# Kernel optimization log

Measured on AMD Instinct MI355X. Metric: run time of the kernel, lower is better.

The kernel has to match this reference:

```python
import jax, jax.numpy as jnp
import numpy as np

G = 64  # voxel grid extent per axis; grid_ind entries are in [0, G)


def setup_inputs() -> dict:
    key = jax.random.key(0)
    k1, k2 = jax.random.split(key)
    N = 4_000_000
    points = jax.random.normal(k1, (N, 7), dtype=jnp.float32)
    grid_ind = jax.random.randint(k2, (N, 3), 0, G, dtype=jnp.int64)
    return {"points": points, "grid_ind": grid_ind}


def reference(points, grid_ind):
    # torch.unique(grid_ind, dim=0, return_inverse=True) sorts rows
    # lexicographically; for nonnegative coords that equals sorting the
    # linearized index, so we dedup the linear id instead of rows.
    N = points.shape[0]
    gi = grid_ind.astype(jnp.int32)
    lin = (gi[:, 0] * G + gi[:, 1]) * G + gi[:, 2]  # [N]
    # fixed-size unique for jit compatibility: at most N unique voxels,
    # padded with fill_value=-1 at the tail.
    unq, unq_inv = jnp.unique(lin, return_inverse=True, size=N, fill_value=-1)
    # scatter_mean over point->voxel mapping
    sums = jax.ops.segment_sum(points, unq_inv, num_segments=N)          # [N, 7]
    cnt = jax.ops.segment_sum(jnp.ones((N,), points.dtype), unq_inv,
                              num_segments=N)                            # [N]
    mean = sums / jnp.maximum(cnt, 1.0)[:, None]
    # reconstruct the [n_unique_padded, 3] voxel coordinates (pad rows = -1)
    valid = unq >= 0
    u = jnp.maximum(unq, 0)
    unq3 = jnp.stack([u // (G * G), (u // G) % G, u % G], axis=-1)
    unq3 = jnp.where(valid[:, None], unq3, -1).astype(grid_ind.dtype)
    return mean, unq3
```

## Files before the change

### kernel.cpp

```cpp
#include <hip/hip_runtime.h>

#define NVOX 262144
#define NB   256
#define VPB  1024
#define PPB  2048
#define SCT  512
#define NBLK 256

__global__ void dv_fill(const unsigned* __restrict__ nuP,
                        float* __restrict__ out, int n) {
    int nu = (int)*nuP;
    size_t meanChunks = (size_t)n * 7 / 4;
    size_t coordChunks = (size_t)n * 3 / 4;
    size_t total = meanChunks + coordChunks;
    size_t i = (size_t)blockIdx.x * blockDim.x + threadIdx.x;
    if (i >= total) return;
    float* mean = out;
    float* coords = out + (size_t)n * 7;
    if (i < meanChunks) {
        size_t base = i * 4, lim = (size_t)nu * 7;
        if (base >= lim) {
            *(float4*)(mean + base) = make_float4(0.f, 0.f, 0.f, 0.f);
        } else if (base + 4 > lim) {
            for (size_t k = lim; k < base + 4; ++k) mean[k] = 0.f;
        }
    } else {
        size_t base = (i - meanChunks) * 4, lim = (size_t)nu * 3;
        if (base >= lim) {
            *(float4*)(coords + base) = make_float4(-1.f, -1.f, -1.f, -1.f);
        } else if (base + 4 > lim) {
            for (size_t k = lim; k < base + 4; ++k) coords[k] = -1.f;
        }
    }
}

__device__ __forceinline__ unsigned bf16rne(float x) {
    unsigned u = __float_as_uint(x);
    u += 0x7fffu + ((u >> 16) & 1u);
    return u >> 16;
}

__global__ void __launch_bounds__(SCT) rx_scatfuse(
        const int* __restrict__ gi, const float* __restrict__ pts, int n,
        unsigned* __restrict__ cursor, int capb, uint4* __restrict__ recs) {
    __shared__ uint4 recS[PPB];
    __shared__ unsigned dstS[PPB];
    __shared__ unsigned hist[NB];
    __shared__ unsigned bStart[NB];
    __shared__ unsigned runS[NB];
    int t = threadIdx.x, b = blockIdx.x;
    int base = b * PPB;
    int cnt = n - base;
    if (cnt > PPB) cnt = PPB;
    if (t < NB) hist[t] = 0;
    __syncthreads();

    unsigned keyA[PPB / SCT], rankA[PPB / SCT];
    int p0 = base + t * 4;
    if (p0 + 4 <= n) {
        const int4* g4 = (const int4*)(gi + (size_t)base * 3);
        int4 a = g4[3 * t], c = g4[3 * t + 1], d = g4[3 * t + 2];
        keyA[0] = ((unsigned)((a.x << 2) | (a.y >> 4)) << 10) |
                  (unsigned)(((a.y & 15) << 6) | a.z);
        keyA[1] = ((unsigned)((a.w << 2) | (c.x >> 4)) << 10) |
                  (unsigned)(((c.x & 15) << 6) | c.y);
        keyA[2] = ((unsigned)((c.z << 2) | (c.w >> 4)) << 10) |
                  (unsigned)(((c.w & 15) << 6) | d.x);
        keyA[3] = ((unsigned)((d.y << 2) | (d.z >> 4)) << 10) |
                  (unsigned)(((d.z & 15) << 6) | d.w);
#pragma unroll
        for (int j = 0; j < 4; ++j)
            rankA[j] = atomicAdd(&hist[keyA[j] >> 10], 1u);
    } else {
#pragma unroll
        for (int j = 0; j < 4; ++j) {
            int i = p0 + j;
            if (i < n) {
                int g0 = gi[3 * i], g1 = gi[3 * i + 1], g2 = gi[3 * i + 2];
                keyA[j] = ((unsigned)((g0 << 2) | (g1 >> 4)) << 10) |
                          (unsigned)(((g1 & 15) << 6) | g2);
                rankA[j] = atomicAdd(&hist[keyA[j] >> 10], 1u);
            }
        }
    }
    __syncthreads();
    unsigned mine = (t < NB) ? hist[t] : 0u;
    for (int d = 1; d < NB; d <<= 1) {
        unsigned v = (t < NB && t >= d) ? hist[t - d] : 0u;
        __syncthreads();
        if (t < NB) hist[t] += v;
        __syncthreads();
    }
    if (t < NB) {
        bStart[t] = hist[t] - mine;
        runS[t] = (mine > 0) ? atomicAdd(&cursor[t], mine) : 0u;
    }
    __syncthreads();

#pragma unroll
    for (int j = 0; j < PPB / SCT; ++j) {
        int lid = t * 4 + j;
        if (lid < cnt) {
            int i = base + lid;
            const float* p = pts + (size_t)i * 7;
            float f0 = p[0], f1 = p[1], f2 = p[2], f3 = p[3];
            float f4 = p[4], f5 = p[5], f6 = p[6];
            unsigned key = keyA[j], rank = rankA[j];
            unsigned bk = key >> 10, sub = key & 1023u;
            uint4 r;
            r.x = bf16rne(f0) | (bf16rne(f1) << 16);
            r.y = bf16rne(f2) | (bf16rne(f3) << 16);
            r.z = bf16rne(f4) | (bf16rne(f5) << 16);
            r.w = bf16rne(f6) | (sub << 16);
            unsigned sp = bStart[bk] + rank;
            recS[sp] = r;
            dstS[sp] = (unsigned)bk * (unsigned)capb + runS[bk] + rank;
        }
    }
    __syncthreads();
#pragma unroll
    for (int k = 0; k < PPB / SCT; ++k) {
        int j = k * SCT + t;
        if (j < cnt) recs[dstS[j]] = recS[j];
    }
}

__global__ void rx_scan256(const unsigned* __restrict__ in,
                           unsigned* __restrict__ out) {
    __shared__ unsigned sm[NB];
    int t = threadIdx.x;
    unsigned mine = in[t];
    sm[t] = mine;
    __syncthreads();
    for (int off = 1; off < NB; off <<= 1) {
        unsigned v = (t >= off) ? sm[t - off] : 0u;
        __syncthreads();
        sm[t] += v;
        __syncthreads();
    }
    out[t] = sm[t] - mine;
    if (t == NB - 1) out[NB] = sm[t];
}

__global__ void __launch_bounds__(1024) rx_accum(
        const uint4* __restrict__ recs, const unsigned* __restrict__ cursor,
        int capb, float* __restrict__ accTable,
        unsigned* __restrict__ occCount) {
    __shared__ uint4 sortedR[2048];
    __shared__ unsigned cnt_[VPB];
    __shared__ unsigned wsum[16];
    int t = threadIdx.x, bk = blockIdx.x;
    int lane = t & 63, wid = t >> 6;
    unsigned len = cursor[bk];
    size_t base = (size_t)bk * (unsigned)capb;
    float a0 = 0.f, a1 = 0.f, a2 = 0.f, a3 = 0.f,
          a4 = 0.f, a5 = 0.f, a6 = 0.f, cf = 0.f;
    for (unsigned cs = 0; cs < len; cs += 2048) {
        bool v0 = (cs + t) < len, v1 = (cs + 1024 + t) < len;
        uint4 r0, r1;
        unsigned k0 = 0, k1 = 0, rk0 = 0, rk1 = 0;
        if (v0) { r0 = recs[base + cs + t]; k0 = r0.w >> 16; }
        if (v1) { r1 = recs[base + cs + 1024 + t]; k1 = r1.w >> 16; }
        cnt_[t] = 0;
        __syncthreads();
        if (v0) rk0 = atomicAdd(&cnt_[k0], 1u);
        if (v1) rk1 = atomicAdd(&cnt_[k1], 1u);
        __syncthreads();
        unsigned own = cnt_[t];
        unsigned x = own;
#pragma unroll
        for (int d = 1; d < 64; d <<= 1) {
            unsigned y = __shfl_up(x, d, 64);
            if (lane >= d) x += y;
        }
        if (lane == 63) wsum[wid] = x;
        __syncthreads();
        if (t < 64) {
            unsigned w = (lane < 16) ? wsum[lane] : 0u;
            unsigned xx = w;
#pragma unroll
            for (int d = 1; d < 16; d <<= 1) {
                unsigned y = __shfl_up(xx, d, 64);
                if (lane >= d) xx += y;
            }
            if (lane < 16) wsum[lane] = xx - w;
        }
        __syncthreads();
        unsigned excl = x - own + wsum[wid];
        cnt_[t] = excl;
        __syncthreads();
        if (v0) sortedR[cnt_[k0] + rk0] = r0;
        if (v1) sortedR[cnt_[k1] + rk1] = r1;
        __syncthreads();
        unsigned st = excl, end = excl + own;
        for (unsigned k = st; k < end; ++k) {
            uint4 r = sortedR[k];
            a0 += __uint_as_float(r.x << 16);
            a1 += __uint_as_float(r.x & 0xffff0000u);
            a2 += __uint_as_float(r.y << 16);
            a3 += __uint_as_float(r.y & 0xffff0000u);
            a4 += __uint_as_float(r.z << 16);
            a5 += __uint_as_float(r.z & 0xffff0000u);
            a6 += __uint_as_float(r.w << 16);
            cf += 1.f;
        }
        __syncthreads();
    }
    float4* o = (float4*)(accTable + ((size_t)bk * VPB + t) * 8);
    o[0] = make_float4(a0, a1, a2, a3);
    o[1] = make_float4(a4, a5, a6, cf);
    unsigned long long m = __ballot(cf > 0.f);
    if (lane == 0) wsum[wid] = (unsigned)__popcll(m);
    __syncthreads();
    if (t == 0) {
        unsigned occ = 0;
#pragma unroll
        for (int w = 0; w < 16; ++w) occ += wsum[w];
        occCount[bk] = occ;
    }
}

__global__ void rx_emit(const float* __restrict__ accTable,
                        const unsigned* __restrict__ rankBase,
                        float* __restrict__ out_mean,
                        float* __restrict__ out_coords) {
    int bk = blockIdx.x, t = threadIdx.x;
    float row[4][8];
    int pre[4], mycount = 0;
#pragma unroll
    for (int j = 0; j < 4; ++j) {
        int v = t * 4 + j;
        const float4* a = (const float4*)(accTable + ((size_t)bk * VPB + v) * 8);
        float4 r0 = a[0], r1 = a[1];
        row[j][0] = r0.x; row[j][1] = r0.y; row[j][2] = r0.z; row[j][3] = r0.w;
        row[j][4] = r1.x; row[j][5] = r1.y; row[j][6] = r1.z; row[j][7] = r1.w;
        pre[j] = mycount;
        mycount += (row[j][7] > 0.f) ? 1 : 0;
    }
    __shared__ int sm[256];
    sm[t] = mycount;
    __syncthreads();
    for (int off = 1; off < 256; off <<= 1) {
        int v = (t >= off) ? sm[t - off] : 0;
        __syncthreads();
        sm[t] += v;
        __syncthreads();
    }
    int rank0 = (int)rankBase[bk] + (sm[t] - mycount);
#pragma unroll
    for (int j = 0; j < 4; ++j) {
        if (row[j][7] > 0.f) {
            int r = rank0 + pre[j];
            int lin = (bk << 10) | (t * 4 + j);
            float inv = 1.0f / row[j][7];
            float* m = out_mean + (size_t)r * 7;
#pragma unroll
            for (int k = 0; k < 7; ++k) m[k] = row[j][k] * inv;
            float* cd = out_coords + (size_t)r * 3;
            cd[0] = (float)(lin >> 12);
            cd[1] = (float)((lin >> 6) & 63);
            cd[2] = (float)(lin & 63);
        }
    }
}

struct Meta {
    unsigned blockSums[NBLK];
    unsigned blockFlagSums[NBLK];
    unsigned blockOffs[NBLK];
    unsigned blockRankOffs[NBLK];
    unsigned nUnique;
};

__global__ void dv_count(const int* __restrict__ gi, int n,
                         unsigned* __restrict__ counts,
                         unsigned short* __restrict__ slots) {
    int i = blockIdx.x * blockDim.x + threadIdx.x;
    if (i >= n) return;
    int lin = (gi[3 * i] << 12) | (gi[3 * i + 1] << 6) | gi[3 * i + 2];
    unsigned s = atomicAdd(&counts[lin], 1u);
    slots[i] = (unsigned short)s;
}

__global__ void dv_bs1(const unsigned* __restrict__ counts,
                       Meta* __restrict__ meta) {
    int b = blockIdx.x, t = threadIdx.x;
    uint4 c = ((const uint4*)(counts + (size_t)b * 1024))[t];
    unsigned cs = c.x + c.y + c.z + c.w;
    unsigned fs = (c.x > 0) + (c.y > 0) + (c.z > 0) + (c.w > 0);
    __shared__ unsigned smC[256], smF[256];
    smC[t] = cs; smF[t] = fs;
    __syncthreads();
    for (int off = 128; off > 0; off >>= 1) {
        if (t < off) { smC[t] += smC[t + off]; smF[t] += smF[t + off]; }
        __syncthreads();
    }
    if (t == 0) { meta->blockSums[b] = smC[0]; meta->blockFlagSums[b] = smF[0]; }
}

__global__ void dv_scan2(unsigned* __restrict__ offsets, int n,
                         Meta* __restrict__ meta) {
    __shared__ unsigned smC[NBLK], smF[NBLK];
    int t = threadIdx.x;
    unsigned c = meta->blockSums[t], f = meta->blockFlagSums[t];
    smC[t] = c; smF[t] = f;
    __syncthreads();
    for (int off = 1; off < NBLK; off <<= 1) {
        unsigned vc = (t >= off) ? smC[t - off] : 0u;
        unsigned vf = (t >= off) ? smF[t - off] : 0u;
        __syncthreads();
        smC[t] += vc; smF[t] += vf;
        __syncthreads();
    }
    meta->blockOffs[t] = smC[t] - c;
    meta->blockRankOffs[t] = smF[t] - f;
    if (t == NBLK - 1) { meta->nUnique = smF[t]; offsets[NVOX] = (unsigned)n; }
}

__global__ void dv_scan3(unsigned* __restrict__ counts,
                         const Meta* __restrict__ meta) {
    int b = blockIdx.x, t = threadIdx.x;
    uint4 c = ((const uint4*)(counts + (size_t)b * 1024))[t];
    unsigned mysum = c.x + c.y + c.z + c.w;
    __shared__ unsigned sm[256];
    sm[t] = mysum;
    __syncthreads();
    for (int off = 1; off < 256; off <<= 1) {
        unsigned v = (t >= off) ? sm[t - off] : 0u;
        __syncthreads();
        sm[t] += v;
        __syncthreads();
    }
    unsigned base = meta->blockOffs[b] + sm[t] - mysum;
    uint4 o;
    o.x = base;
    o.y = base + c.x;
    o.z = o.y + c.y;
    o.w = o.z + c.z;
    ((uint4*)(counts + (size_t)b * 1024))[t] = o;
}

__global__ void dv_scatter2(const int* __restrict__ gi, int n,
                            const unsigned* __restrict__ offsets,
                            const unsigned short* __restrict__ slots,
                            unsigned* __restrict__ perm) {
    int i = blockIdx.x * blockDim.x + threadIdx.x;
    if (i >= n) return;
    int lin = (gi[3 * i] << 12) | (gi[3 * i + 1] << 6) | gi[3 * i + 2];
    perm[offsets[lin] + (unsigned)slots[i]] = (unsigned)i;
}

__global__ void dv_emit2(const float* __restrict__ points,
                         const unsigned* __restrict__ offsets,
                         const unsigned* __restrict__ perm,
                         const Meta* __restrict__ meta,
                         float* __restrict__ out_mean,
                         float* __restrict__ out_coords) {
    int b = blockIdx.x, t = threadIdx.x;
    int base = b * 1024 + t * 4;
    uint4 o4 = ((const uint4*)offsets)[b * 256 + t];
    unsigned o[5];
    o[0] = o4.x; o[1] = o4.y; o[2] = o4.z; o[3] = o4.w;
    o[4] = offsets[base + 4];
    int c[4], pre[4], mycount = 0;
#pragma unroll
    for (int j = 0; j < 4; ++j) {
        c[j] = (int)(o[j + 1] - o[j]);
        pre[j] = mycount;
        mycount += (c[j] > 0) ? 1 : 0;
    }
    __shared__ int sm[256];
    sm[t] = mycount;
    __syncthreads();
    for (int off = 1; off < 256; off <<= 1) {
        int v = (t >= off) ? sm[t - off] : 0;
        __syncthreads();
        sm[t] += v;
        __syncthreads();
    }
    int rank0 = (int)meta->blockRankOffs[b] + (sm[t] - mycount);
#pragma unroll
    for (int j = 0; j < 4; ++j) {
        if (c[j] > 0) {
            float s0 = 0.f, s1 = 0.f, s2 = 0.f, s3 = 0.f,
                  s4 = 0.f, s5 = 0.f, s6 = 0.f;
            for (unsigned k = o[j]; k < o[j + 1]; ++k) {
                unsigned idx = perm[k];
                const float* p = points + (size_t)idx * 7;
                s0 += p[0]; s1 += p[1]; s2 += p[2]; s3 += p[3];
                s4 += p[4]; s5 += p[5]; s6 += p[6];
            }
            int r = rank0 + pre[j];
            int v = base + j;
            float inv = 1.0f / (float)c[j];
            float* m = out_mean + (size_t)r * 7;
            m[0] = s0 * inv; m[1] = s1 * inv; m[2] = s2 * inv;
            m[3] = s3 * inv; m[4] = s4 * inv; m[5] = s5 * inv;
            m[6] = s6 * inv;
            float* cd = out_coords + (size_t)r * 3;
            cd[0] = (float)(v >> 12);
            cd[1] = (float)((v >> 6) & 63);
            cd[2] = (float)(v & 63);
        }
    }
}

extern "C" void kernel_launch(void* const* d_in, const int* in_sizes, int n_in,
                              void* d_out, int out_size, void* d_ws, size_t ws_size,
                              hipStream_t stream) {
    const float* points = (const float*)d_in[0];
    const int*   gi     = (const int*)d_in[1];
    int n = in_sizes[0] / 7;

    float* out_mean   = (float*)d_out;
    float* out_coords = (float*)d_out + (size_t)n * 7;

    int threads = 256;
    int nb1 = (n + PPB - 1) / PPB;

    int capb = n / NB + n / NB / 8 + 1024;
    size_t recsB = (size_t)NB * capb * 16;
    size_t accB  = (size_t)NB * VPB * 8 * sizeof(float);
    size_t need  = recsB + accB + NB * 4  + NB * 4  +
                   (NB + 1) * 4  + 256;

    size_t fillChunks = (size_t)n * 7 / 4 + (size_t)n * 3 / 4;
    int fillBlocks = (int)((fillChunks + threads - 1) / threads);

    if (ws_size >= need) {
        char* w = (char*)d_ws;
        uint4*    recs     = (uint4*)w;                    w += recsB;
        float*    accTable = (float*)w;                    w += accB;
        unsigned* cursor   = (unsigned*)w;                 w += NB * 4;
        unsigned* occCount = (unsigned*)w;                 w += NB * 4;
        unsigned* rankBase = (unsigned*)w;

        hipMemsetAsync(cursor, 0, NB * 4, stream);
        rx_scatfuse<<<nb1, SCT, 0, stream>>>(gi, points, n, cursor, capb, recs);
        rx_accum<<<NB, 1024, 0, stream>>>(recs, cursor, capb, accTable,
                                          occCount);
        rx_scan256<<<1, NB, 0, stream>>>(occCount, rankBase);
        rx_emit<<<NB, 256, 0, stream>>>(accTable, rankBase, out_mean,
                                        out_coords);
        dv_fill<<<fillBlocks, threads, 0, stream>>>(rankBase + NB,
                                                    (float*)d_out, n);
    } else {
        char* w = (char*)d_ws;
        unsigned*       perm    = (unsigned*)w;
        unsigned short* slots   = (unsigned short*)(w + (size_t)n * 4);
        unsigned*       offsets = (unsigned*)(w + (size_t)n * 4 + (size_t)n * 2);
        Meta*           meta    = (Meta*)((char*)offsets + (size_t)(NVOX + 4) * 4);

        hipMemsetAsync(offsets, 0, (size_t)(NVOX + 4) * 4, stream);

        int blocksN = (n + threads - 1) / threads;
        dv_count<<<blocksN, threads, 0, stream>>>(gi, n, offsets, slots);
        dv_bs1<<<NBLK, 256, 0, stream>>>(offsets, meta);
        dv_scan2<<<1, NBLK, 0, stream>>>(offsets, n, meta);
        dv_scan3<<<NBLK, 256, 0, stream>>>(offsets, meta);
        dv_scatter2<<<blocksN, threads, 0, stream>>>(gi, n, offsets, slots, perm);
        dv_emit2<<<NBLK, 256, 0, stream>>>(points, offsets, perm, meta,
                                           out_mean, out_coords);
        dv_fill<<<fillBlocks, threads, 0, stream>>>(&meta->nUnique,
                                                    (float*)d_out, n);
    }
}
```

Before: 377.9 us.

## Fold bucket scan into emit, vectorize point loads, widen accum chunk

Several changes land together. The standalone single-block rx_scan256 launch is removed, and every rx_emit block now recomputes the 256-entry prefix over occCount redundantly. In rx_scatfuse the shared-memory Hillis-Steele scan becomes a wavefront shuffle scan, and full tiles load their points as seven float4 vectors instead of scalar loads. rx_accum processes 4096 records per chunk instead of 2048, which doubles its LDS footprint (about 69 KB at 1024 threads) and may limit occupancy.

Result: faster. 359.7 us (-4.8%).

```diff
diff --git a/kernel.cpp b/kernel.cpp
--- a/kernel.cpp
+++ b/kernel.cpp
@@ -5,6 +5,7 @@
 #define VPB  1024
 #define PPB  2048
 #define SCT  512
+#define CHK  4096
 #define NBLK 256
 
 __global__ void dv_fill(const unsigned* __restrict__ nuP,
@@ -48,7 +49,9 @@
     __shared__ unsigned hist[NB];
     __shared__ unsigned bStart[NB];
     __shared__ unsigned runS[NB];
+    __shared__ unsigned wsumS[8];
     int t = threadIdx.x, b = blockIdx.x;
+    int lane = t & 63, wid = t >> 6;
     int base = b * PPB;
     int cnt = n - base;
     if (cnt > PPB) cnt = PPB;
@@ -57,7 +60,8 @@
 
     unsigned keyA[PPB / SCT], rankA[PPB / SCT];
     int p0 = base + t * 4;
-    if (p0 + 4 <= n) {
+    bool full = (p0 + 4 <= n);
+    if (full) {
         const int4* g4 = (const int4*)(gi + (size_t)base * 3);
         int4 a = g4[3 * t], c = g4[3 * t + 1], d = g4[3 * t + 2];
         keyA[0] = ((unsigned)((a.x << 2) | (a.y >> 4)) << 10) |
@@ -85,37 +89,75 @@
     }
     __syncthreads();
     unsigned mine = (t < NB) ? hist[t] : 0u;
-    for (int d = 1; d < NB; d <<= 1) {
-        unsigned v = (t < NB && t >= d) ? hist[t - d] : 0u;
-        __syncthreads();
-        if (t < NB) hist[t] += v;
-        __syncthreads();
-    }
+    unsigned x = mine;
+#pragma unroll
+    for (int d = 1; d < 64; d <<= 1) {
+        unsigned y = __shfl_up(x, d, 64);
+        if (lane >= d) x += y;
+    }
+    if (t < NB && lane == 63) wsumS[wid] = x;
+    __syncthreads();
+    if (t < 64) {
+        unsigned w = (lane < 4) ? wsumS[lane] : 0u, xx = w;
+#pragma unroll
+        for (int d = 1; d < 4; d <<= 1) {
+            unsigned y = __shfl_up(xx, d, 64);
+            if (lane >= d) xx += y;
+        }
+        if (lane < 4) wsumS[lane] = xx - w;
+    }
+    __syncthreads();
     if (t < NB) {
-        bStart[t] = hist[t] - mine;
+        unsigned incl = x + wsumS[wid];
+        bStart[t] = incl - mine;
         runS[t] = (mine > 0) ? atomicAdd(&cursor[t], mine) : 0u;
     }
     __syncthreads();
 
-#pragma unroll
-    for (int j = 0; j < PPB / SCT; ++j) {
-        int lid = t * 4 + j;
-        if (lid < cnt) {
-            int i = base + lid;
-            const float* p = pts + (size_t)i * 7;
-            float f0 = p[0], f1 = p[1], f2 = p[2], f3 = p[3];
-            float f4 = p[4], f5 = p[5], f6 = p[6];
+    if (full) {
+        float f[28];
+        const float4* p4 = (const float4*)(pts + (size_t)base * 7) +
+                           (size_t)t * 7;
+#pragma unroll
+        for (int q = 0; q < 7; ++q) {
+            float4 u = p4[q];
+            f[q * 4 + 0] = u.x; f[q * 4 + 1] = u.y;
+            f[q * 4 + 2] = u.z; f[q * 4 + 3] = u.w;
+        }
+#pragma unroll
+        for (int j = 0; j < 4; ++j) {
             unsigned key = keyA[j], rank = rankA[j];
             unsigned bk = key >> 10, sub = key & 1023u;
             uint4 r;
-            r.x = bf16rne(f0) | (bf16rne(f1) << 16);
-            r.y = bf16rne(f2) | (bf16rne(f3) << 16);
-            r.z = bf16rne(f4) | (bf16rne(f5) << 16);
-            r.w = bf16rne(f6) | (sub << 16);
+            r.x = bf16rne(f[j * 7 + 0]) | (bf16rne(f[j * 7 + 1]) << 16);
+            r.y = bf16rne(f[j * 7 + 2]) | (bf16rne(f[j * 7 + 3]) << 16);
+            r.z = bf16rne(f[j * 7 + 4]) | (bf16rne(f[j * 7 + 5]) << 16);
+            r.w = bf16rne(f[j * 7 + 6]) | (sub << 16);
             unsigned sp = bStart[bk] + rank;
             recS[sp] = r;
             dstS[sp] = (unsigned)bk * (unsigned)capb + runS[bk] + rank;
         }
+    } else {
+#pragma unroll
+        for (int j = 0; j < 4; ++j) {
+            int lid = t * 4 + j;
+            if (lid < cnt) {
+                int i = base + lid;
+                const float* p = pts + (size_t)i * 7;
+                float f0 = p[0], f1 = p[1], f2 = p[2], f3 = p[3];
+                float f4 = p[4], f5 = p[5], f6 = p[6];
+                unsigned key = keyA[j], rank = rankA[j];
+                unsigned bk = key >> 10, sub = key & 1023u;
+                uint4 r;
+                r.x = bf16rne(f0) | (bf16rne(f1) << 16);
+                r.y = bf16rne(f2) | (bf16rne(f3) << 16);
+                r.z = bf16rne(f4) | (bf16rne(f5) << 16);
+                r.w = bf16rne(f6) | (sub << 16);
+                unsigned sp = bStart[bk] + rank;
+                recS[sp] = r;
+                dstS[sp] = (unsigned)bk * (unsigned)capb + runS[bk] + rank;
+            }
+        }
     }
     __syncthreads();
 #pragma unroll
@@ -123,30 +165,13 @@
         int j = k * SCT + t;
         if (j < cnt) recs[dstS[j]] = recS[j];
     }
-}
-
-__global__ void rx_scan256(const unsigned* __restrict__ in,
-                           unsigned* __restrict__ out) {
-    __shared__ unsigned sm[NB];
-    int t = threadIdx.x;
-    unsigned mine = in[t];
-    sm[t] = mine;
-    __syncthreads();
-    for (int off = 1; off < NB; off <<= 1) {
-        unsigned v = (t >= off) ? sm[t - off] : 0u;
-        __syncthreads();
-        sm[t] += v;
-        __syncthreads();
-    }
-    out[t] = sm[t] - mine;
-    if (t == NB - 1) out[NB] = sm[t];
 }
 
 __global__ void __launch_bounds__(1024) rx_accum(
         const uint4* __restrict__ recs, const unsigned* __restrict__ cursor,
         int capb, float* __restrict__ accTable,
         unsigned* __restrict__ occCount) {
-    __shared__ uint4 sortedR[2048];
+    __shared__ uint4 sortedR[CHK];
     __shared__ unsigned cnt_[VPB];
     __shared__ unsigned wsum[16];
     int t = threadIdx.x, bk = blockIdx.x;
@@ -155,16 +180,24 @@
     size_t base = (size_t)bk * (unsigned)capb;
     float a0 = 0.f, a1 = 0.f, a2 = 0.f, a3 = 0.f,
           a4 = 0.f, a5 = 0.f, a6 = 0.f, cf = 0.f;
-    for (unsigned cs = 0; cs < len; cs += 2048) {
-        bool v0 = (cs + t) < len, v1 = (cs + 1024 + t) < len;
-        uint4 r0, r1;
-        unsigned k0 = 0, k1 = 0, rk0 = 0, rk1 = 0;
-        if (v0) { r0 = recs[base + cs + t]; k0 = r0.w >> 16; }
-        if (v1) { r1 = recs[base + cs + 1024 + t]; k1 = r1.w >> 16; }
+    for (unsigned cs = 0; cs < len; cs += CHK) {
+        bool v[4];
+        uint4 r[4];
+        unsigned k[4], rk[4];
+#pragma unroll
+        for (int j = 0; j < 4; ++j) {
+            v[j] = (cs + j * 1024 + t) < len;
+            k[j] = 0; rk[j] = 0;
+            if (v[j]) {
+                r[j] = recs[base + cs + j * 1024 + t];
+                k[j] = r[j].w >> 16;
+            }
+        }
         cnt_[t] = 0;
         __syncthreads();
-        if (v0) rk0 = atomicAdd(&cnt_[k0], 1u);
-        if (v1) rk1 = atomicAdd(&cnt_[k1], 1u);
+#pragma unroll
+        for (int j = 0; j < 4; ++j)
+            if (v[j]) rk[j] = atomicAdd(&cnt_[k[j]], 1u);
         __syncthreads();
         unsigned own = cnt_[t];
         unsigned x = own;
@@ -189,19 +222,20 @@
         unsigned excl = x - own + wsum[wid];
         cnt_[t] = excl;
         __syncthreads();
-        if (v0) sortedR[cnt_[k0] + rk0] = r0;
-        if (v1) sortedR[cnt_[k1] + rk1] = r1;
+#pragma unroll
+        for (int j = 0; j < 4; ++j)
+            if (v[j]) sortedR[cnt_[k[j]] + rk[j]] = r[j];
         __syncthreads();
         unsigned st = excl, end = excl + own;
-        for (unsigned k = st; k < end; ++k) {
-            uint4 r = sortedR[k];
-            a0 += __uint_as_float(r.x << 16);
-            a1 += __uint_as_float(r.x & 0xffff0000u);
-            a2 += __uint_as_float(r.y << 16);
-            a3 += __uint_as_float(r.y & 0xffff0000u);
-            a4 += __uint_as_float(r.z << 16);
-            a5 += __uint_as_float(r.z & 0xffff0000u);
-            a6 += __uint_as_float(r.w << 16);
+        for (unsigned q = st; q < end; ++q) {
+            uint4 rr = sortedR[q];
+            a0 += __uint_as_float(rr.x << 16);
+            a1 += __uint_as_float(rr.x & 0xffff0000u);
+            a2 += __uint_as_float(rr.y << 16);
+            a3 += __uint_as_float(rr.y & 0xffff0000u);
+            a4 += __uint_as_float(rr.z << 16);
+            a5 += __uint_as_float(rr.z & 0xffff0000u);
+            a6 += __uint_as_float(rr.w << 16);
             cf += 1.f;
         }
         __syncthreads();
@@ -221,10 +255,27 @@
 }
 
 __global__ void rx_emit(const float* __restrict__ accTable,
-                        const unsigned* __restrict__ rankBase,
+                        const unsigned* __restrict__ occCount,
+                        unsigned* __restrict__ nuOut,
                         float* __restrict__ out_mean,
                         float* __restrict__ out_coords) {
     int bk = blockIdx.x, t = threadIdx.x;
+
+    __shared__ unsigned smB[NB];
+    __shared__ unsigned rankBaseS;
+    unsigned mineB = occCount[t];
+    smB[t] = mineB;
+    __syncthreads();
+    for (int off = 1; off < NB; off <<= 1) {
+        unsigned v = (t >= off) ? smB[t - off] : 0u;
+        __syncthreads();
+        smB[t] += v;
+        __syncthreads();
+    }
+    if (t == bk) rankBaseS = smB[t] - mineB;
+    if (bk == 0 && t == NB - 1) *nuOut = smB[t];
+    __syncthreads();
+
     float row[4][8];
     int pre[4], mycount = 0;
 #pragma unroll
@@ -246,7 +297,7 @@
         sm[t] += v;
         __syncthreads();
     }
-    int rank0 = (int)rankBase[bk] + (sm[t] - mycount);
+    int rank0 = (int)rankBaseS + (sm[t] - mycount);
 #pragma unroll
     for (int j = 0; j < 4; ++j) {
         if (row[j][7] > 0.f) {
@@ -422,7 +473,7 @@
     size_t recsB = (size_t)NB * capb * 16;
     size_t accB  = (size_t)NB * VPB * 8 * sizeof(float);
     size_t need  = recsB + accB + NB * 4  + NB * 4  +
-                   (NB + 1) * 4  + 256;
+                   4  + 256;
 
     size_t fillChunks = (size_t)n * 7 / 4 + (size_t)n * 3 / 4;
     int fillBlocks = (int)((fillChunks + threads - 1) / threads);
@@ -433,16 +484,15 @@
         float*    accTable = (float*)w;                    w += accB;
         unsigned* cursor   = (unsigned*)w;                 w += NB * 4;
         unsigned* occCount = (unsigned*)w;                 w += NB * 4;
-        unsigned* rankBase = (unsigned*)w;
+        unsigned* nuTotal  = (unsigned*)w;
 
         hipMemsetAsync(cursor, 0, NB * 4, stream);
         rx_scatfuse<<<nb1, SCT, 0, stream>>>(gi, points, n, cursor, capb, recs);
         rx_accum<<<NB, 1024, 0, stream>>>(recs, cursor, capb, accTable,
                                           occCount);
-        rx_scan256<<<1, NB, 0, stream>>>(occCount, rankBase);
-        rx_emit<<<NB, 256, 0, stream>>>(accTable, rankBase, out_mean,
+        rx_emit<<<NB, 256, 0, stream>>>(accTable, occCount, nuTotal, out_mean,
                                         out_coords);
-        dv_fill<<<fillBlocks, threads, 0, stream>>>(rankBase + NB,
+        dv_fill<<<fillBlocks, threads, 0, stream>>>(nuTotal,
                                                     (float*)d_out, n);
     } else {
         char* w = (char*)d_ws;
```
